# Kernel optimization log

Hardware: AMD Instinct MI355X
Metric: run time of the kernel (lower is better)

The kernel has to match this reference:

```python
import jax, jax.numpy as jnp
import numpy as np

B = 4          # graphs
N = 8192       # coarse nodes (2048/graph)
M = 65536      # fine (skip) nodes (16384/graph)
E = 131072     # edges (32768/graph)
T = 16         # global tokens per graph
F_IN = 16      # dim of x and x_skip (concat -> in_channels = 32)
HID, OUT = 32, 16
ED, GD, EMB, H = 3, 1024, 64, 4
K = 3


def _make_pe(t, d):
    # PositionalEncoding buffer (sin/cos), deterministic constant
    position = np.arange(t, dtype=np.float32)[:, None]
    div = np.exp(np.arange(0, d, 2, dtype=np.float32) * (-np.log(10000.0) / d))
    pe = np.zeros((t, d), dtype=np.float32)
    pe[:, 0::2] = np.sin(position * div)
    pe[:, 1::2] = np.cos(position * div)
    return jnp.asarray(pe)


def setup_inputs():
    key = jax.random.key(0)
    ks = jax.random.split(key, 30)
    n, m, e = N // B, M // B, E // B
    inp = {}
    inp['x'] = jax.random.normal(ks[0], (N, F_IN), jnp.float32)
    inp['pos'] = jax.random.normal(ks[1], (N, 3), jnp.float32)
    inp['batch'] = jnp.repeat(jnp.arange(B), n)
    inp['x_skip'] = jax.random.normal(ks[2], (M, F_IN), jnp.float32)
    inp['pos_skip'] = jax.random.normal(ks[3], (M, 3), jnp.float32)
    inp['batch_skip'] = jnp.repeat(jnp.arange(B), m)
    off = jnp.repeat(jnp.arange(B) * m, e)
    inp['edge_index'] = jax.random.randint(ks[4], (2, E), 0, m) + off[None, :]
    inp['global_token'] = jax.random.normal(ks[5], (B * T, GD), jnp.float32)
    def lin(k, o, i, s):
        return jax.random.normal(k, (o, i), jnp.float32) * s
    inp['Wq_w'] = lin(ks[6], EMB, ED, 0.3); inp['Wq_b'] = jnp.zeros((EMB,), jnp.float32)
    inp['Wk_w'] = lin(ks[7], EMB, GD, 0.03); inp['Wk_b'] = jnp.zeros((EMB,), jnp.float32)
    inp['Wv_w'] = lin(ks[8], EMB, GD, 0.03); inp['Wv_b'] = jnp.zeros((EMB,), jnp.float32)
    inp['in_proj_w'] = lin(ks[9], 3 * EMB, EMB, 0.125); inp['in_proj_b'] = jnp.zeros((3 * EMB,), jnp.float32)
    inp['out_w'] = lin(ks[10], EMB, EMB, 0.125); inp['out_b'] = jnp.zeros((EMB,), jnp.float32)
    dims = [(2 * F_IN, HID), (HID, HID), (HID, OUT)]
    for i, (ci, co) in enumerate(dims):
        inp[f'nn_w{i}'] = lin(ks[11 + 3 * i], ci * co, ED + EMB, 0.05)
        inp[f'nn_b{i}'] = jnp.zeros((ci * co,), jnp.float32)
        inp[f'root{i}'] = jax.random.normal(ks[12 + 3 * i], (ci, co), jnp.float32) * (1.0 / np.sqrt(ci))
        inp[f'bias{i}'] = jnp.zeros((co,), jnp.float32)
    return inp


def reference(x, pos, batch, x_skip, pos_skip, batch_skip, edge_index, global_token,
              Wq_w, Wq_b, Wk_w, Wk_b, Wv_w, Wv_b, in_proj_w, in_proj_b, out_w, out_b,
              nn_w0, nn_b0, root0, bias0, nn_w1, nn_b1, root1, bias1, nn_w2, nn_b2, root2, bias2):
    # ---- knn_interpolate (k=3, inverse squared-distance weighting) ----
    # graphs are equal-sized by construction so per-graph knn == batched knn
    pos_b = pos.reshape(B, -1, 3)
    posk_b = pos_skip.reshape(B, -1, 3)
    d2 = ((posk_b ** 2).sum(-1)[:, :, None] + (pos_b ** 2).sum(-1)[:, None, :]
          - 2.0 * jnp.einsum('bmc,bnc->bmn', posk_b, pos_b))  # [B,m,n]
    neg, idx = jax.lax.top_k(-d2, K)                           # [B,m,K]
    w = 1.0 / jnp.maximum(-neg, 1e-16)
    x_b = x.reshape(B, -1, x.shape[-1])
    feats = jnp.take_along_axis(x_b[:, None, :, :], idx[:, :, :, None], axis=2)  # [B,m,K,F]
    xf = ((w[..., None] * feats).sum(2) / w.sum(2)[..., None]).reshape(M, -1)

    src, dst = edge_index[0], edge_index[1]
    pseudo = pos_skip[dst] - pos_skip[src]                     # patch_size is None
    edge_pos = (0.5 * (pos_skip[dst] + pos_skip[src])).reshape(B, -1, 3)
    gt = global_token.reshape(B, -1, global_token.shape[-1])
    pe = _make_pe(gt.shape[1], EMB)
    Q = edge_pos @ Wq_w.T + Wq_b                               # [B,Eb,EMB]
    Kt = gt @ Wk_w.T + Wk_b + pe                               # dropout in eval = identity
    Vt = gt @ Wv_w.T + Wv_b + pe
    # ---- MultiheadAttention (batch_first) ----
    wq, wk, wv = jnp.split(in_proj_w, 3, axis=0)
    bq, bk, bv = jnp.split(in_proj_b, 3, axis=0)
    hd = EMB // H
    def heads(t, w_, b_):
        t = t @ w_.T + b_
        return t.reshape(t.shape[0], t.shape[1], H, hd).transpose(0, 2, 1, 3)
    q, k_, v = heads(Q, wq, bq), heads(Kt, wk, bk), heads(Vt, wv, bv)
    att = jax.nn.softmax(jnp.einsum('bhqd,bhkd->bhqk', q, k_) / np.sqrt(hd).astype(np.float32), axis=-1)
    o = jnp.einsum('bhqk,bhkd->bhqd', att, v).transpose(0, 2, 1, 3).reshape(B, -1, EMB)
    o = o @ out_w.T + out_b
    pseudo = jnp.concatenate([pseudo, o.reshape(-1, EMB)], axis=-1)  # [E, 3+64]

    # ---- NNConv stack (gather -> edge MLP -> per-edge matmul -> scatter mean) ----
    h = jnp.concatenate([xf, x_skip], axis=1)                  # [M, 32]
    ones = jnp.ones((E,), jnp.float32)
    cnt = jnp.maximum(jax.ops.segment_sum(ones, dst, num_segments=M), 1.0)[:, None]
    for nw, nb, rt, bs in ((nn_w0, nn_b0, root0, bias0),
                           (nn_w1, nn_b1, root1, bias1),
                           (nn_w2, nn_b2, root2, bias2)):
        ci, co = rt.shape
        we = jax.nn.relu(pseudo @ nw.T + nb).reshape(E, ci, co)  # MLP (BN at default eval stats ~ identity)
        msg = jnp.einsum('ei,eio->eo', h[src], we)               # [E, co]
        aggr = jax.ops.segment_sum(msg, dst, num_segments=M) / cnt
        h = jax.nn.relu(aggr + h @ rt + bs)                      # drop_act=False -> relu every layer
    return h, pos_skip, batch_skip
```

## Files before the change

### kernel.cpp

```cpp
#include <hip/hip_runtime.h>
#include <math.h>

#define NB    4
#define NN    8192
#define MM    65536
#define EE    131072
#define NPG   2048

typedef short short8 __attribute__((ext_vector_type(8)));
typedef float f32x4  __attribute__((ext_vector_type(4)));

static __device__ inline unsigned short f2b(float f) {
    unsigned u = __float_as_uint(f);
    u += 0x7fffu + ((u >> 16) & 1u);
    return (unsigned short)(u >> 16);
}
static __device__ inline unsigned f2b_pack(float a, float b) {
    unsigned x = __float_as_uint(a); x += 0x7fffu + ((x >> 16) & 1u);
    unsigned y = __float_as_uint(b); y += 0x7fffu + ((y >> 16) & 1u);
    return (x >> 16) | (y & 0xffff0000u);
}
static __device__ inline short8 bc8(uint4 v) {
    union { uint4 u; short8 s; } c; c.u = v; return c.s;
}

__global__ __launch_bounds__(256)
void k_knn(const float4* __restrict__ cpre, const float* __restrict__ pos,
           const float* __restrict__ pos_skip,
           const float* __restrict__ x, const float* __restrict__ x_skip,
           const int* __restrict__ batch_skip,
           float* __restrict__ h0, float* __restrict__ out_pos,
           float* __restrict__ out_batch)
{
    __shared__ float  pk[4][64][3];
    __shared__ float  wFin[64][3];
    __shared__ int    iFin[64][3];

    int tid = threadIdx.x;
    int g = blockIdx.x >> 8;
    int cbase = g * NPG;
    int node = tid & 63;
    int slice = tid >> 6;
    int fbase = blockIdx.x * 64;
    int f = fbase + node;
    float fx = pos_skip[f * 3 + 0], fy = pos_skip[f * 3 + 1], fz = pos_skip[f * 3 + 2];

    int slice_u = __builtin_amdgcn_readfirstlane(slice);
    const float4* cw = cpre + (size_t)cbase + (size_t)slice_u * 512;

    float k0 = 3.4028235e38f, k1 = 3.4028235e38f, k2 = 3.4028235e38f;
#pragma unroll 8
    for (int l = 0; l < 512; ++l) {
        float4 cc = cw[l];
        float d = fmaf(cc.x, fx, cc.w);
        d = fmaf(cc.y, fy, d);
        d = fmaf(cc.z, fz, d);
        float key = __uint_as_float((__float_as_uint(d) & 0xFFFFFE00u) | (unsigned)l);
        float t = fmaxf(k1, key);
        k2 = fminf(k2, t);
        k1 = __builtin_amdgcn_fmed3f(k0, k1, key);
        k0 = fminf(k0, key);
    }
    pk[slice][node][0] = k0; pk[slice][node][1] = k1; pk[slice][node][2] = k2;
    __syncthreads();

    if (tid < 64) {
        int n = tid;
        int fn = fbase + n;
        float gx = pos_skip[fn * 3 + 0], gy = pos_skip[fn * 3 + 1], gz = pos_skip[fn * 3 + 2];
        float gq = gx * gx + gy * gy + gz * gz;
        unsigned long long m0 = ~0ull, m1 = ~0ull, m2 = ~0ull;
#pragma unroll
        for (int s = 0; s < 4; ++s)
#pragma unroll
            for (int r = 0; r < 3; ++r) {
                unsigned key = __float_as_uint(pk[s][n][r]);
                int c = cbase + s * 512 + (int)(key & 511u);
                float px = pos[c * 3 + 0];
                float py = pos[c * 3 + 1];
                float pz = pos[c * 3 + 2];
                float d = gq + (px * px + py * py + pz * pz);
                d = fmaf(-2.f * px, gx, d);
                d = fmaf(-2.f * py, gy, d);
                d = fmaf(-2.f * pz, gz, d);
                d = fmaxf(d, 0.f);
                unsigned long long kk = ((unsigned long long)__float_as_uint(d) << 32) | (unsigned)c;
                unsigned long long t1 = m0 > kk ? m0 : kk; m0 = m0 < kk ? m0 : kk;
                unsigned long long t2 = m1 > t1 ? m1 : t1; m1 = m1 < t1 ? m1 : t1;
                m2 = m2 < t2 ? m2 : t2;
            }
        float d0 = __uint_as_float((unsigned)(m0 >> 32));
        float d1 = __uint_as_float((unsigned)(m1 >> 32));
        float d2 = __uint_as_float((unsigned)(m2 >> 32));
        float w0 = 1.f / fmaxf(d0, 1e-16f);
        float w1 = 1.f / fmaxf(d1, 1e-16f);
        float w2 = 1.f / fmaxf(d2, 1e-16f);
        float inv = 1.f / (w0 + w1 + w2);
        wFin[n][0] = w0 * inv; wFin[n][1] = w1 * inv; wFin[n][2] = w2 * inv;
        iFin[n][0] = (int)(m0 & 0xffffffffull);
        iFin[n][1] = (int)(m1 & 0xffffffffull);
        iFin[n][2] = (int)(m2 & 0xffffffffull);
        out_pos[fn * 3 + 0] = gx; out_pos[fn * 3 + 1] = gy; out_pos[fn * 3 + 2] = gz;
        out_batch[fn] = (float)batch_skip[fn];
    }
    __syncthreads();

    int n2 = tid >> 2, part = tid & 3;
    int f2 = fbase + n2;
    float4* h04 = (float4*)(h0 + (size_t)f2 * 32);
    if (part < 2) {
        const float4* x4 = (const float4*)x;
        float w0 = wFin[n2][0], w1 = wFin[n2][1], w2 = wFin[n2][2];
        int a0 = iFin[n2][0] * 4, a1 = iFin[n2][1] * 4, a2 = iFin[n2][2] * 4;
#pragma unroll
        for (int j = 0; j < 2; ++j) {
            int cj = part * 2 + j;
            float4 v0 = x4[a0 + cj], v1 = x4[a1 + cj], v2 = x4[a2 + cj];
            float4 r;
            r.x = w0 * v0.x + w1 * v1.x + w2 * v2.x;
            r.y = w0 * v0.y + w1 * v1.y + w2 * v2.y;
            r.z = w0 * v0.z + w1 * v1.z + w2 * v2.z;
            r.w = w0 * v0.w + w1 * v1.w + w2 * v2.w;
            h04[cj] = r;
        }
    } else {
        const float4* xs4 = (const float4*)x_skip;
#pragma unroll
        for (int j = 0; j < 2; ++j) {
            int cj = (part - 2) * 2 + j;
            h04[4 + cj] = xs4[f2 * 4 + cj];
        }
    }
}

__global__ __launch_bounds__(128)
void k_tokens1(const float* __restrict__ gt,
               const float* __restrict__ Wk_w, const float* __restrict__ Wk_b,
               const float* __restrict__ Wv_w, const float* __restrict__ Wv_b,
               const float* __restrict__ pos, float4* __restrict__ cpre,
               float* __restrict__ KtVt)
{
    int cgid = blockIdx.x * 128 + threadIdx.x;
    {
        float px = pos[cgid * 3 + 0];
        float py = pos[cgid * 3 + 1];
        float pz = pos[cgid * 3 + 2];
        cpre[cgid] = make_float4(-2.f * px, -2.f * py, -2.f * pz,
                                 px * px + py * py + pz * pz);
    }
    int b = blockIdx.x >> 4;
    int t = blockIdx.x & 15;
    int which = threadIdx.x >> 6;
    int d = threadIdx.x & 63;
    const float* W = which ? Wv_w : Wk_w;
    const float* bias = which ? Wv_b : Wk_b;
    const float4* row = (const float4*)(gt + (size_t)(b * 16 + t) * 1024);
    const float4* wr = (const float4*)(W + (size_t)d * 1024);
    float acc = 0.f;
    for (int c = 0; c < 256; ++c) {
        float4 a = row[c], w = wr[c];
        acc += a.x * w.x; acc += a.y * w.y; acc += a.z * w.z; acc += a.w * w.w;
    }
    int i2 = d >> 1;
    float dv = expf((float)(2 * i2) * (-0.14391156831212787f));
    float ang = (float)t * dv;
    float pe = (d & 1) ? cosf(ang) : sinf(ang);
    KtVt[((size_t)(b * 2 + which) * 16 + t) * 64 + d] = acc + bias[d] + pe;
}

__global__ __launch_bounds__(256)
void k_tokens2(const float* __restrict__ KtVt,
               const float* __restrict__ in_proj_w, const float* __restrict__ in_proj_b,
               const float* __restrict__ out_w,
               const float* __restrict__ Wq_w, const float* __restrict__ Wq_b,
               float* __restrict__ Mfold, uint4* __restrict__ v2fG)
{
    int b = blockIdx.x;
    int tid = threadIdx.x;
    __shared__ float KtL[1024], VtL[1024], vv[1024], kproj[1024];
    __shared__ float v2L[4096];
    __shared__ float qWs[192], qbs[64];
    for (int idx = tid; idx < 1024; idx += 256) {
        KtL[idx] = KtVt[(size_t)(b * 2 + 0) * 1024 + idx];
        VtL[idx] = KtVt[(size_t)(b * 2 + 1) * 1024 + idx];
    }
    __syncthreads();
    for (int idx = tid; idx < 2048; idx += 256) {
        int which = idx >> 10; int td = idx & 1023; int t = td >> 6; int j = td & 63;
        int r = (which ? 128 : 64) + j;
        const float* w = in_proj_w + (size_t)r * 64;
        const float* src = which ? VtL : KtL;
        float acc = in_proj_b[r];
#pragma unroll 8
        for (int dd = 0; dd < 64; ++dd) acc += src[t * 64 + dd] * w[dd];
        if (which) vv[t * 64 + j] = acc;
        else kproj[t * 64 + j] = acc;
    }
    for (int idx = tid; idx < 192; idx += 256) {
        int c = idx >> 6; int j = idx & 63;
        float acc = 0.f;
        for (int dd = 0; dd < 64; ++dd) acc += in_proj_w[(size_t)j * 64 + dd] * Wq_w[dd * 3 + c];
        qWs[c * 64 + j] = acc;
    }
    for (int j = tid; j < 64; j += 256) {
        float acc = in_proj_b[j];
        for (int dd = 0; dd < 64; ++dd) acc += in_proj_w[(size_t)j * 64 + dd] * Wq_b[dd];
        qbs[j] = acc;
    }
    __syncthreads();
    for (int idx = tid; idx < 4096; idx += 256) {
        int jo = idx & 63; int th2 = idx >> 6; int h = th2 & 3; int t = th2 >> 2;
        float acc = 0.f;
#pragma unroll
        for (int dd = 0; dd < 16; ++dd)
            acc += vv[t * 64 + h * 16 + dd] * out_w[(size_t)jo * 64 + h * 16 + dd];
        v2L[(t * 4 + h) * 64 + jo] = acc;
    }
    {
        int th = tid >> 2, c = tid & 3;
        int t = th >> 2, h = th & 3;
        float acc = 0.f;
#pragma unroll
        for (int dd = h * 16; dd < h * 16 + 16; ++dd) {
            float w = (c == 0) ? qWs[dd] : (c == 1) ? qWs[64 + dd]
                    : (c == 2) ? qWs[128 + dd] : qbs[dd];
            acc += w * kproj[t * 64 + dd];
        }
        Mfold[((size_t)b * 64 + th) * 4 + c] = 0.25f * acc;
    }
    __syncthreads();
    for (int it = tid; it < 512; it += 256) {
        int lane = it & 63, fi = it >> 6;
        int mi = fi >> 1, step = fi & 1;
        int outd = mi * 16 + (lane & 15);
        int th0 = step * 32 + (lane >> 4) * 8;
        uint4 v;
        v.x = f2b_pack(v2L[(th0 + 0) * 64 + outd], v2L[(th0 + 1) * 64 + outd]);
        v.y = f2b_pack(v2L[(th0 + 2) * 64 + outd], v2L[(th0 + 3) * 64 + outd]);
        v.z = f2b_pack(v2L[(th0 + 4) * 64 + outd], v2L[(th0 + 5) * 64 + outd]);
        v.w = f2b_pack(v2L[(th0 + 6) * 64 + outd], v2L[(th0 + 7) * 64 + outd]);
        v2fG[((size_t)b * 8 + fi) * 64 + lane] = v;
    }
}

__global__ __launch_bounds__(256)
void k_edge_attn(const float* __restrict__ ps, const int* __restrict__ ei,
                 const float* __restrict__ Mfold, const uint4* __restrict__ v2f,
                 const float* __restrict__ ob,
                 unsigned short* __restrict__ Pf, float* __restrict__ cnt)
{
    __shared__ unsigned attL[4 * 64 * 34];
    int tid = threadIdx.x;
    int wave = tid >> 6, lane = tid & 63, q = lane >> 4, c15 = lane & 15;
    int g = blockIdx.x >> 7;
    int e = blockIdx.x * 256 + tid;
    int s = ei[e], d = ei[EE + e];
    atomicAdd(&cnt[d], 1.f);
    float sx = ps[s * 3], sy = ps[s * 3 + 1], sz = ps[s * 3 + 2];
    float dx = ps[d * 3], dy = ps[d * 3 + 1], dz = ps[d * 3 + 2];
    float px = dx - sx, py = dy - sy, pz = dz - sz;
    float ex = 0.5f * (dx + sx), ey = 0.5f * (dy + sy), ez = 0.5f * (dz + sz);

    const float4* Mg = (const float4*)Mfold + (size_t)g * 64;
    float sc[64];
#pragma unroll
    for (int th = 0; th < 64; ++th) {
        float4 m = Mg[th];
        sc[th] = ex * m.x + ey * m.y + ez * m.z + m.w;
    }
#pragma unroll
    for (int h = 0; h < 4; ++h) {
        float mx = sc[h];
#pragma unroll
        for (int t = 1; t < 16; ++t) mx = fmaxf(mx, sc[t * 4 + h]);
        float ssum = 0.f;
#pragma unroll
        for (int t = 0; t < 16; ++t) {
            float eo = expf(sc[t * 4 + h] - mx);
            sc[t * 4 + h] = eo; ssum += eo;
        }
        float inv = 1.f / ssum;
#pragma unroll
        for (int t = 0; t < 16; ++t) sc[t * 4 + h] *= inv;
    }
    unsigned* slab = attL + wave * 64 * 34;
#pragma unroll
    for (int k = 0; k < 16; ++k) {
        uint2 v;
        v.x = f2b_pack(sc[4 * k + 0], sc[4 * k + 1]);
        v.y = f2b_pack(sc[4 * k + 2], sc[4 * k + 3]);
        *(uint2*)&slab[lane * 34 + 2 * k] = v;
    }
    __syncthreads();

    uint4 v2a[4][2];
#pragma unroll
    for (int mi = 0; mi < 4; ++mi)
#pragma unroll
        for (int st = 0; st < 2; ++st)
            v2a[mi][st] = v2f[((size_t)g * 8 + mi * 2 + st) * 64 + lane];

    f32x4 acc[4][4];
#pragma unroll
    for (int mi = 0; mi < 4; ++mi)
#pragma unroll
        for (int nt = 0; nt < 4; ++nt) acc[mi][nt] = (f32x4){0.f, 0.f, 0.f, 0.f};

#pragma unroll
    for (int nt = 0; nt < 4; ++nt) {
        const unsigned* rb = &slab[(nt * 16 + c15) * 34];
        uint4 b0 = *(const uint4*)&rb[q * 4];
        uint4 b1 = *(const uint4*)&rb[16 + q * 4];
#pragma unroll
        for (int mi = 0; mi < 4; ++mi) {
            acc[mi][nt] = __builtin_amdgcn_mfma_f32_16x16x32_bf16(bc8(v2a[mi][0]), bc8(b0), acc[mi][nt], 0, 0, 0);
            acc[mi][nt] = __builtin_amdgcn_mfma_f32_16x16x32_bf16(bc8(v2a[mi][1]), bc8(b1), acc[mi][nt], 0, 0, 0);
        }
    }
    __syncthreads();

    float4 obv[4];
#pragma unroll
    for (int mi = 0; mi < 4; ++mi) obv[mi] = *(const float4*)(ob + mi * 16 + q * 4);
#pragma unroll
    for (int mi = 0; mi < 4; ++mi)
#pragma unroll
        for (int nt = 0; nt < 4; ++nt) {
            f32x4 a = acc[mi][nt];
            uint2 v;
            v.x = f2b_pack(a[0] + obv[mi].x, a[1] + obv[mi].y);
            v.y = f2b_pack(a[2] + obv[mi].z, a[3] + obv[mi].w);
            *(uint2*)&slab[(nt * 16 + c15) * 34 + mi * 8 + q * 2] = v;
        }
    __syncthreads();

    uint4* Pf4 = (uint4*)Pf;
#pragma unroll
    for (int et = 0; et < 4; ++et) {
        int etg = blockIdx.x * 16 + wave * 4 + et;
#pragma unroll
        for (int st = 0; st < 2; ++st) {
            uint4 w = *(const uint4*)&slab[(et * 16 + c15) * 34 + st * 16 + q * 4];
            Pf4[((size_t)etg * 3 + st) * 64 + lane] = w;
        }
    }
    int et2 = e >> 4, eL = e & 15;
    size_t tb = ((size_t)(et2 * 3 + 2) * 64 + 0 * 16 + eL) * 8;
    uint2 t0; t0.x = f2b_pack(px, py); t0.y = f2b_pack(pz, 1.0f);
    *(uint2*)(Pf + tb) = t0;
    uint2 z2; z2.x = 0u; z2.y = 0u;
    *(uint2*)(Pf + tb + 4) = z2;
#pragma unroll
    for (int quad = 1; quad < 4; ++quad) {
        size_t zb = ((size_t)(et2 * 3 + 2) * 64 + quad * 16 + eL) * 8;
        uint4 z4; z4.x = 0u; z4.y = 0u; z4.z = 0u; z4.w = 0u;
        *(uint4*)(Pf + zb) = z4;
    }
}

static __device__ inline void repack_one(const float* __restrict__ nw,
                                         const float* __restrict__ nb,
                                         unsigned short* __restrict__ Wf, int idx)
{
    int jj = idx & 7;
    int lane = (idx >> 3) & 63;
    int rest = idx >> 9;
    int s = rest % 3;
    int jt = rest / 3;
    int j = jt * 16 + (lane & 15);
    int k = s * 32 + (lane >> 4) * 8 + jj;
    float v;
    if (k < 64)       v = nw[(size_t)j * 67 + 3 + k];
    else if (k < 67)  v = nw[(size_t)j * 67 + (k - 64)];
    else if (k == 67) v = nb[j];
    else              v = 0.f;
    Wf[idx] = f2b(v);
}

__global__ __launch_bounds__(256)
void k_repackAll(const float* __restrict__ nw0, const float* __restrict__ nb0,
                 const float* __restrict__ nw1, const float* __restrict__ nb1,
                 const float* __restrict__ nw2, const float* __restrict__ nb2,
                 unsigned short* __restrict__ Wf0, unsigned short* __restrict__ Wf1,
                 unsigned short* __restrict__ Wf2)
{
    int idx = blockIdx.x * 256 + threadIdx.x;
    if (idx < 98304)        repack_one(nw0, nb0, Wf0, idx);
    else if (idx < 196608)  repack_one(nw1, nb1, Wf1, idx - 98304);
    else                    repack_one(nw2, nb2, Wf2, idx - 196608);
}

template<int CO>
__global__ __launch_bounds__(256, 4)
void k_conv_mfma(const uint4* __restrict__ Pf, const float* __restrict__ hin,
                 const int* __restrict__ ei, const uint4* __restrict__ Wf,
                 float* __restrict__ aggr)
{
    __shared__ float hL[128 * 36];
    __shared__ int sL[128];
    __shared__ int dL[128];
    constexpr int REDSZ = (CO == 16) ? 2 * 64 * 17 : 4;
    __shared__ float red[REDSZ];

    int tid = threadIdx.x;
    int e0 = blockIdx.x * 128;
    if (tid < 128) sL[tid] = ei[e0 + tid];
    else           dL[tid - 128] = ei[EE + e0 + (tid - 128)];
    __syncthreads();
    for (int idx = tid; idx < 1024; idx += 256) {
        int row = idx >> 3, c = idx & 7;
        const float4* hr = (const float4*)(hin + (size_t)sL[row] * 32);
        *(float4*)&hL[row * 36 + c * 4] = hr[c];
    }
    __syncthreads();

    int wave = tid >> 6, lane = tid & 63, quad = lane >> 4, col = lane & 15;
    int group = wave >> 1, half = wave & 1;

    uint4 a[4][3];
    int et0 = blockIdx.x * 8 + group * 4;
#pragma unroll
    for (int st = 0; st < 4; ++st)
#pragma unroll
        for (int s = 0; s < 3; ++s)
            a[st][s] = Pf[((size_t)(et0 + st) * 3 + s) * 64 + lane];

    float msg[4][4];
#pragma unroll
    for (int st = 0; st < 4; ++st)
#pragma unroll
        for (int r = 0; r < 4; ++r) msg[st][r] = 0.f;

    int ibase = (CO == 32) ? 0 : half * 16;
    constexpr int NI2 = (CO == 32) ? 16 : 8;

    for (int i2 = 0; i2 < NI2; ++i2) {
        float2 hv2[4][4];
#pragma unroll
        for (int st = 0; st < 4; ++st)
#pragma unroll
            for (int r = 0; r < 4; ++r)
                hv2[st][r] = *(const float2*)&hL[(group * 64 + st * 16 + quad * 4 + r) * 36
                                                 + ibase + i2 * 2];
#pragma unroll
        for (int ii = 0; ii < 2; ++ii) {
            int i = ibase + i2 * 2 + ii;
            int jt = (CO == 32) ? (i * 2 + half) : i;
            uint4 b0 = Wf[((size_t)jt * 3 + 0) * 64 + lane];
            uint4 b1 = Wf[((size_t)jt * 3 + 1) * 64 + lane];
            uint4 b2 = Wf[((size_t)jt * 3 + 2) * 64 + lane];
#pragma unroll
            for (int st = 0; st < 4; ++st) {
                f32x4 c = {0.f, 0.f, 0.f, 0.f};
                c = __builtin_amdgcn_mfma_f32_16x16x32_bf16(bc8(a[st][0]), bc8(b0), c, 0, 0, 0);
                c = __builtin_amdgcn_mfma_f32_16x16x32_bf16(bc8(a[st][1]), bc8(b1), c, 0, 0, 0);
                c = __builtin_amdgcn_mfma_f32_16x16x32_bf16(bc8(a[st][2]), bc8(b2), c, 0, 0, 0);
#pragma unroll
                for (int r = 0; r < 4; ++r) {
                    float hv = ii ? hv2[st][r].y : hv2[st][r].x;
                    msg[st][r] += hv * fmaxf(c[r], 0.f);
                }
            }
        }
    }

    if (CO == 32) {
#pragma unroll
        for (int st = 0; st < 4; ++st)
#pragma unroll
            for (int r = 0; r < 4; ++r) {
                int dv = dL[group * 64 + st * 16 + quad * 4 + r];
                atomicAdd(&aggr[(size_t)dv * 32 + half * 16 + col], msg[st][r]);
            }
    } else {
        if (half == 1) {
#pragma unroll
            for (int st = 0; st < 4; ++st)
#pragma unroll
                for (int r = 0; r < 4; ++r)
                    red[group * 64 * 17 + lane * 17 + st * 4 + r] = msg[st][r];
        }
        __syncthreads();
        if (half == 0) {
#pragma unroll
            for (int st = 0; st < 4; ++st)
#pragma unroll
                for (int r = 0; r < 4; ++r) {
                    float m = msg[st][r] + red[group * 64 * 17 + lane * 17 + st * 4 + r];
                    int dv = dL[group * 64 + st * 16 + quad * 4 + r];
                    atomicAdd(&aggr[(size_t)dv * 16 + col], m);
                }
        }
    }
}

template<int CO>
__global__ __launch_bounds__(256)
void k_update(float* __restrict__ aggr, const float* __restrict__ cnt,
              const float* __restrict__ hin, const float* __restrict__ root,
              const float* __restrict__ bias, float* __restrict__ hout)
{
    __shared__ float rL[32 * CO];
    __shared__ float bL[CO];
    int tid = threadIdx.x;
    for (int idx = tid; idx < 32 * CO; idx += 256) rL[idx] = root[idx];
    if (tid < CO) bL[tid] = bias[tid];
    __syncthreads();
    int gid = blockIdx.x * 256 + tid;
    int v = gid / CO;
    int o = gid % CO;
    float acc = aggr[gid] / fmaxf(cnt[v], 1.f) + bL[o];
    aggr[gid] = 0.f;
    const float* hr = hin + (size_t)v * 32;
#pragma unroll
    for (int i = 0; i < 32; ++i) acc += hr[i] * rL[i * CO + o];
    hout[gid] = fmaxf(acc, 0.f);
}

extern "C" void kernel_launch(void* const* d_in, const int* in_sizes, int n_in,
                              void* d_out, int out_size, void* d_ws, size_t ws_size,
                              hipStream_t stream)
{
    const float* x          = (const float*)d_in[0];
    const float* pos        = (const float*)d_in[1];
    const float* x_skip     = (const float*)d_in[3];
    const float* pos_skip   = (const float*)d_in[4];
    const int*   batch_skip = (const int*)  d_in[5];
    const int*   ei         = (const int*)  d_in[6];
    const float* gt         = (const float*)d_in[7];
    const float* Wq_w       = (const float*)d_in[8];
    const float* Wq_b       = (const float*)d_in[9];
    const float* Wk_w       = (const float*)d_in[10];
    const float* Wk_b       = (const float*)d_in[11];
    const float* Wv_w       = (const float*)d_in[12];
    const float* Wv_b       = (const float*)d_in[13];
    const float* in_proj_w  = (const float*)d_in[14];
    const float* in_proj_b  = (const float*)d_in[15];
    const float* out_w      = (const float*)d_in[16];
    const float* out_b      = (const float*)d_in[17];
    const float* nn_w0 = (const float*)d_in[18]; const float* nn_b0 = (const float*)d_in[19];
    const float* root0 = (const float*)d_in[20]; const float* bias0 = (const float*)d_in[21];
    const float* nn_w1 = (const float*)d_in[22]; const float* nn_b1 = (const float*)d_in[23];
    const float* root1 = (const float*)d_in[24]; const float* bias1 = (const float*)d_in[25];
    const float* nn_w2 = (const float*)d_in[26]; const float* nn_b2 = (const float*)d_in[27];
    const float* root2 = (const float*)d_in[28]; const float* bias2 = (const float*)d_in[29];

    char* wsb = (char*)d_ws;
    size_t off = 0;
    auto carve = [&](size_t bytes) { char* p = wsb + off; off += (bytes + 255) & ~(size_t)255; return p; };
    float* aggr = (float*)carve((size_t)MM * 32 * 4);
    float* cnt  = (float*)carve((size_t)MM * 4);
    float* hA   = (float*)carve((size_t)MM * 32 * 4);
    float* hB   = (float*)carve((size_t)MM * 32 * 4);
    unsigned short* Pf  = (unsigned short*)carve((size_t)EE * 96 * 2);
    unsigned short* Wf0 = (unsigned short*)carve((size_t)1024 * 96 * 2);
    unsigned short* Wf1 = (unsigned short*)carve((size_t)1024 * 96 * 2);
    unsigned short* Wf2 = (unsigned short*)carve((size_t)512 * 96 * 2);
    float* Mfold = (float*)carve((size_t)NB * 64 * 4 * 4);
    uint4* v2f   = (uint4*)carve((size_t)NB * 8 * 64 * 16);
    float* KtVt  = (float*)carve((size_t)NB * 2 * 16 * 64 * 4);
    float4* cpre = (float4*)carve((size_t)NN * 16);

    float* h_final   = (float*)d_out;
    float* out_pos   = (float*)d_out + (size_t)MM * 16;
    float* out_batch = (float*)d_out + (size_t)MM * 19;

    hipMemsetAsync(aggr, 0, ((size_t)MM * 32 + MM) * sizeof(float), stream);

    k_tokens1<<<64, 128, 0, stream>>>(gt, Wk_w, Wk_b, Wv_w, Wv_b, pos, cpre, KtVt);
    k_tokens2<<<NB, 256, 0, stream>>>(KtVt, in_proj_w, in_proj_b, out_w, Wq_w, Wq_b,
                                      Mfold, v2f);
    k_knn<<<MM / 64, 256, 0, stream>>>(cpre, pos, pos_skip, x, x_skip, batch_skip,
                                       hA, out_pos, out_batch);
    k_edge_attn<<<EE / 256, 256, 0, stream>>>(pos_skip, ei, Mfold, v2f, out_b,
                                              Pf, cnt);
    k_repackAll<<<960, 256, 0, stream>>>(nn_w0, nn_b0, nn_w1, nn_b1, nn_w2, nn_b2,
                                         Wf0, Wf1, Wf2);

    k_conv_mfma<32><<<EE / 128, 256, 0, stream>>>((const uint4*)Pf, hA, ei, (const uint4*)Wf0, aggr);
    k_update<32><<<(MM * 32) / 256, 256, 0, stream>>>(aggr, cnt, hA, root0, bias0, hB);
    k_conv_mfma<32><<<EE / 128, 256, 0, stream>>>((const uint4*)Pf, hB, ei, (const uint4*)Wf1, aggr);
    k_update<32><<<(MM * 32) / 256, 256, 0, stream>>>(aggr, cnt, hB, root1, bias1, hA);
    k_conv_mfma<16><<<EE / 128, 256, 0, stream>>>((const uint4*)Pf, hA, ei, (const uint4*)Wf2, aggr);
    k_update<16><<<(MM * 16) / 256, 256, 0, stream>>>(aggr, cnt, hA, root2, bias2, h_final);
}
```

Measured before the change: 369.9 us.

## Two-level clustered kNN search with LDS-staged coarse points

Rewrites the kNN kernel as a two-level search. Coarse points are staged in shared memory, and each thread computes per-cluster minimum distances for two fine nodes across clusters of 32 points. It then keeps the three best clusters and runs an exact top-3 search only inside them, merging the results across threads. This replaces the per-point top-3 insertion over 512 candidates plus global position rereads, but adds extra barriers and more shared memory per block. The quantized cluster keys could also break near-ties differently than before.

Result: faster. 345.8 us (-6.5%).

```diff
diff --git a/kernel.cpp b/kernel.cpp
--- a/kernel.cpp
+++ b/kernel.cpp
@@ -24,67 +24,127 @@
     union { uint4 u; short8 s; } c; c.u = v; return c.s;
 }
 
-__global__ __launch_bounds__(256)
-void k_knn(const float4* __restrict__ cpre, const float* __restrict__ pos,
-           const float* __restrict__ pos_skip,
+__global__ __launch_bounds__(512)
+void k_knn(const float4* __restrict__ cpre, const float* __restrict__ pos_skip,
            const float* __restrict__ x, const float* __restrict__ x_skip,
            const int* __restrict__ batch_skip,
            float* __restrict__ h0, float* __restrict__ out_pos,
            float* __restrict__ out_batch)
 {
-    __shared__ float  pk[4][64][3];
-    __shared__ float  wFin[64][3];
-    __shared__ int    iFin[64][3];
+    __shared__ float4 cp[2048];
+    __shared__ float  pk[8][128][3];
+    __shared__ int    chosen[128][3];
+    __shared__ unsigned long long fin[3][128][3];
+    __shared__ float  wFin[128][3];
+    __shared__ int    iFin[128][3];
 
     int tid = threadIdx.x;
-    int g = blockIdx.x >> 8;
+    int g = blockIdx.x >> 7;
     int cbase = g * NPG;
-    int node = tid & 63;
-    int slice = tid >> 6;
-    int fbase = blockIdx.x * 64;
-    int f = fbase + node;
-    float fx = pos_skip[f * 3 + 0], fy = pos_skip[f * 3 + 1], fz = pos_skip[f * 3 + 2];
-
-    int slice_u = __builtin_amdgcn_readfirstlane(slice);
-    const float4* cw = cpre + (size_t)cbase + (size_t)slice_u * 512;
-
-    float k0 = 3.4028235e38f, k1 = 3.4028235e38f, k2 = 3.4028235e38f;
+    int fbase = blockIdx.x * 128;
+    int wave = tid >> 6;
+    int lane = tid & 63;
+
+    for (int c = tid; c < 2048; c += 512) cp[c] = cpre[cbase + c];
+
+    int nA = lane, nB = lane + 64;
+    float fxA = pos_skip[(fbase + nA) * 3 + 0];
+    float fyA = pos_skip[(fbase + nA) * 3 + 1];
+    float fzA = pos_skip[(fbase + nA) * 3 + 2];
+    float fxB = pos_skip[(fbase + nB) * 3 + 0];
+    float fyB = pos_skip[(fbase + nB) * 3 + 1];
+    float fzB = pos_skip[(fbase + nB) * 3 + 2];
+    __syncthreads();
+
+    const float4* cps = cp + wave * 256;
+    float k0A = 3.4028235e38f, k1A = 3.4028235e38f, k2A = 3.4028235e38f;
+    float k0B = 3.4028235e38f, k1B = 3.4028235e38f, k2B = 3.4028235e38f;
+#pragma unroll
+    for (int j = 0; j < 8; ++j) {
+        float mA = 3.4028235e38f, mB = 3.4028235e38f;
 #pragma unroll 8
-    for (int l = 0; l < 512; ++l) {
-        float4 cc = cw[l];
-        float d = fmaf(cc.x, fx, cc.w);
-        d = fmaf(cc.y, fy, d);
-        d = fmaf(cc.z, fz, d);
-        float key = __uint_as_float((__float_as_uint(d) & 0xFFFFFE00u) | (unsigned)l);
-        float t = fmaxf(k1, key);
-        k2 = fminf(k2, t);
-        k1 = __builtin_amdgcn_fmed3f(k0, k1, key);
-        k0 = fminf(k0, key);
-    }
-    pk[slice][node][0] = k0; pk[slice][node][1] = k1; pk[slice][node][2] = k2;
-    __syncthreads();
-
-    if (tid < 64) {
+        for (int i = 0; i < 32; ++i) {
+            float4 cc = cps[j * 32 + i];
+            float dA = fmaf(cc.x, fxA, cc.w);
+            dA = fmaf(cc.y, fyA, dA);
+            dA = fmaf(cc.z, fzA, dA);
+            mA = fminf(mA, dA);
+            float dB = fmaf(cc.x, fxB, cc.w);
+            dB = fmaf(cc.y, fyB, dB);
+            dB = fmaf(cc.z, fzB, dB);
+            mB = fminf(mB, dB);
+        }
+        unsigned cid = (unsigned)(wave * 8 + j);
+        float keyA = __uint_as_float((__float_as_uint(mA) & 0xFFFFFFC0u) | cid);
+        float tA = fmaxf(k1A, keyA);
+        k2A = fminf(k2A, tA);
+        k1A = __builtin_amdgcn_fmed3f(k0A, k1A, keyA);
+        k0A = fminf(k0A, keyA);
+        float keyB = __uint_as_float((__float_as_uint(mB) & 0xFFFFFFC0u) | cid);
+        float tB = fmaxf(k1B, keyB);
+        k2B = fminf(k2B, tB);
+        k1B = __builtin_amdgcn_fmed3f(k0B, k1B, keyB);
+        k0B = fminf(k0B, keyB);
+    }
+    pk[wave][nA][0] = k0A; pk[wave][nA][1] = k1A; pk[wave][nA][2] = k2A;
+    pk[wave][nB][0] = k0B; pk[wave][nB][1] = k1B; pk[wave][nB][2] = k2B;
+    __syncthreads();
+
+    if (tid < 128) {
         int n = tid;
+        float m0 = 3.4028235e38f, m1 = 3.4028235e38f, m2 = 3.4028235e38f;
+#pragma unroll
+        for (int s = 0; s < 8; ++s)
+#pragma unroll
+            for (int r = 0; r < 3; ++r) {
+                float k = pk[s][n][r];
+                float t = fmaxf(m1, k);
+                m2 = fminf(m2, t);
+                m1 = __builtin_amdgcn_fmed3f(m0, m1, k);
+                m0 = fminf(m0, k);
+            }
+        chosen[n][0] = (int)(__float_as_uint(m0) & 63u);
+        chosen[n][1] = (int)(__float_as_uint(m1) & 63u);
+        chosen[n][2] = (int)(__float_as_uint(m2) & 63u);
+    }
+    __syncthreads();
+
+    if ((tid >> 7) < 3) {
+        int n = tid & 127;
+        int j = tid >> 7;
+        int cid = chosen[n][j];
         int fn = fbase + n;
         float gx = pos_skip[fn * 3 + 0], gy = pos_skip[fn * 3 + 1], gz = pos_skip[fn * 3 + 2];
         float gq = gx * gx + gy * gy + gz * gz;
         unsigned long long m0 = ~0ull, m1 = ~0ull, m2 = ~0ull;
-#pragma unroll
-        for (int s = 0; s < 4; ++s)
+#pragma unroll 4
+        for (int i = 0; i < 32; ++i) {
+            int ii = (i + lane) & 31;
+            float4 cc = cp[cid * 32 + ii];
+            float d = gq + cc.w;
+            d = fmaf(cc.x, gx, d);
+            d = fmaf(cc.y, gy, d);
+            d = fmaf(cc.z, gz, d);
+            d = fmaxf(d, 0.f);
+            unsigned c = (unsigned)(cbase + cid * 32 + ii);
+            unsigned long long kk = ((unsigned long long)__float_as_uint(d) << 32) | c;
+            unsigned long long t1 = m0 > kk ? m0 : kk; m0 = m0 < kk ? m0 : kk;
+            unsigned long long t2 = m1 > t1 ? m1 : t1; m1 = m1 < t1 ? m1 : t1;
+            m2 = m2 < t2 ? m2 : t2;
+        }
+        fin[j][n][0] = m0; fin[j][n][1] = m1; fin[j][n][2] = m2;
+    }
+    __syncthreads();
+
+    if (tid < 128) {
+        int n = tid;
+        int fn = fbase + n;
+        unsigned long long m0 = ~0ull, m1 = ~0ull, m2 = ~0ull;
+#pragma unroll
+        for (int j = 0; j < 3; ++j)
 #pragma unroll
             for (int r = 0; r < 3; ++r) {
-                unsigned key = __float_as_uint(pk[s][n][r]);
-                int c = cbase + s * 512 + (int)(key & 511u);
-                float px = pos[c * 3 + 0];
-                float py = pos[c * 3 + 1];
-                float pz = pos[c * 3 + 2];
-                float d = gq + (px * px + py * py + pz * pz);
-                d = fmaf(-2.f * px, gx, d);
-                d = fmaf(-2.f * py, gy, d);
-                d = fmaf(-2.f * pz, gz, d);
-                d = fmaxf(d, 0.f);
-                unsigned long long kk = ((unsigned long long)__float_as_uint(d) << 32) | (unsigned)c;
+                unsigned long long kk = fin[j][n][r];
                 unsigned long long t1 = m0 > kk ? m0 : kk; m0 = m0 < kk ? m0 : kk;
                 unsigned long long t2 = m1 > t1 ? m1 : t1; m1 = m1 < t1 ? m1 : t1;
                 m2 = m2 < t2 ? m2 : t2;
@@ -100,6 +160,7 @@
         iFin[n][0] = (int)(m0 & 0xffffffffull);
         iFin[n][1] = (int)(m1 & 0xffffffffull);
         iFin[n][2] = (int)(m2 & 0xffffffffull);
+        float gx = pos_skip[fn * 3 + 0], gy = pos_skip[fn * 3 + 1], gz = pos_skip[fn * 3 + 2];
         out_pos[fn * 3 + 0] = gx; out_pos[fn * 3 + 1] = gy; out_pos[fn * 3 + 2] = gz;
         out_batch[fn] = (float)batch_skip[fn];
     }
@@ -570,8 +631,8 @@
     k_tokens1<<<64, 128, 0, stream>>>(gt, Wk_w, Wk_b, Wv_w, Wv_b, pos, cpre, KtVt);
     k_tokens2<<<NB, 256, 0, stream>>>(KtVt, in_proj_w, in_proj_b, out_w, Wq_w, Wq_b,
                                       Mfold, v2f);
-    k_knn<<<MM / 64, 256, 0, stream>>>(cpre, pos, pos_skip, x, x_skip, batch_skip,
-                                       hA, out_pos, out_batch);
+    k_knn<<<MM / 128, 512, 0, stream>>>(cpre, pos_skip, x, x_skip, batch_skip,
+                                        hA, out_pos, out_batch);
     k_edge_attn<<<EE / 256, 256, 0, stream>>>(pos_skip, ei, Mfold, v2f, out_b,
                                               Pf, cnt);
     k_repackAll<<<960, 256, 0, stream>>>(nn_w0, nn_b0, nn_w1, nn_b1, nn_w2, nn_b2,
```
